# Optimization experiments

Measured on AMD Instinct MI355X. Metric: run time of the kernel, lower is better.

The kernel has to match this reference:

```python
import jax, jax.numpy as jnp
import numpy as np

NPERSEG = 512
STEP = 256
NSEG = 9            # frames for L=2048 with boundary='zeros', padded=True
NFREQ = 257
NUM_FILTER = 2
PI = 3.1415926      # same constant as source

_win = 0.5 * (1.0 - jnp.cos(2.0 * jnp.pi * jnp.arange(NPERSEG, dtype=jnp.float32) / NPERSEG))  # periodic hann (scipy get_window('hann'))
_win_sum = 256.0    # sum of periodic hann, exact


def _stft(x):
    # x: (B, D, L) real -> scipy.signal.stft(..., nperseg=512, noverlap=256) => (B, D, 257, 9)
    xp = jnp.pad(x, ((0, 0), (0, 0), (STEP, STEP)))  # boundary='zeros'
    idx = jnp.arange(NSEG)[:, None] * STEP + jnp.arange(NPERSEG)[None, :]
    frames = xp[..., idx] * _win                     # (B,D,9,512)
    Z = jnp.fft.rfft(frames, axis=-1) / _win_sum     # scaling='spectrum'
    return jnp.swapaxes(Z, -1, -2)                   # (B,D,257,9)


def _istft(Z):
    # Z: (B,D,257,9) complex -> (B,D,2048) real (scipy.signal.istft inverse)
    xs = jnp.fft.irfft(jnp.swapaxes(Z, -1, -2) * _win_sum, n=NPERSEG, axis=-1) * _win  # (B,D,9,512)
    total = NPERSEG + (NSEG - 1) * STEP  # 2560
    idx = (jnp.arange(NSEG)[:, None] * STEP + jnp.arange(NPERSEG)[None, :]).reshape(-1)
    B, D = Z.shape[0], Z.shape[1]
    x = jnp.zeros((B, D, total), xs.dtype).at[..., idx].add(xs.reshape(B, D, -1))
    norm = jnp.zeros((total,), jnp.float32).at[idx].add(jnp.tile(_win ** 2, NSEG))
    x = x / jnp.where(norm > 1e-10, norm, 1.0)
    return x[..., STEP:total - STEP]  # trim boundary padding -> length 2048


def _cplx(p):
    return p[..., 0] + 1j * p[..., 1]  # torch.view_as_complex


def _filter(x, length, bank):
    # x: (B,S,D) complex; bank: (K,S,D,2). power = x*x/length (complex square, as in source)
    power = x * x / length
    k = jnp.arange(NUM_FILTER, dtype=jnp.float32)
    coef = jnp.cos((2.0 * (k + 1.0) - 1.0) * PI / 2.0 * NUM_FILTER)  # matches source precedence
    return jnp.sum(power[None] * _cplx(bank)[:, None] * coef[:, None, None, None], axis=0)


def _ln(x, g, b):
    m = jnp.mean(x, -1, keepdims=True)
    v = jnp.mean((x - m) ** 2, -1, keepdims=True)
    return (x - m) * jax.lax.rsqrt(v + 1e-5) * g + b


def _addnorm(x, g1, b1, w1, bb1, w2, bb2, g2, b2):
    x = _ln(x, g1, b1)
    h = jax.nn.gelu(x @ w1.T + bb1, approximate=False)  # torch GELU (exact)
    return _ln(h @ w2.T + bb2 + x, g2, b2)


def setup_inputs() -> dict:
    key = jax.random.key(0)
    ks = jax.random.split(key, 12)
    B, D = 8, 768
    d = {}
    d['ecg'] = jax.random.normal(ks[0], (B, 2048, D), jnp.float32)
    d['image'] = jax.random.normal(ks[1], (B, 196, D), jnp.float32)
    d['ecg_filter_bank'] = jax.random.normal(ks[2], (2, 2313, D, 2), jnp.float32)
    d['cxr_filter_bank'] = jax.random.normal(ks[3], (2, 99, D, 2), jnp.float32)
    d['gate_sel'] = jax.random.normal(ks[4], (99, D, 2), jnp.float32)
    d['gate_w'] = jax.random.normal(ks[5], (D, D), jnp.float32) * 0.02
    d['gate_b'] = jnp.zeros((D,), jnp.float32)
    for i, p in enumerate(['e', 'c']):
        d[p + '_ln1_g'] = jnp.ones((D,), jnp.float32)
        d[p + '_ln1_b'] = jnp.zeros((D,), jnp.float32)
        d[p + '_w1'] = jax.random.normal(ks[6 + 2 * i], (D, D), jnp.float32) * 0.02
        d[p + '_b1'] = jnp.zeros((D,), jnp.float32)
        d[p + '_w2'] = jax.random.normal(ks[7 + 2 * i], (D, D), jnp.float32) * 0.02
        d[p + '_b2'] = jnp.zeros((D,), jnp.float32)
        d[p + '_ln2_g'] = jnp.ones((D,), jnp.float32)
        d[p + '_ln2_b'] = jnp.zeros((D,), jnp.float32)
    return d


def reference(ecg, image, ecg_filter_bank, cxr_filter_bank, gate_sel, gate_w, gate_b,
              e_ln1_g, e_ln1_b, e_w1, e_b1, e_w2, e_b2, e_ln2_g, e_ln2_b,
              c_ln1_g, c_ln1_b, c_w1, c_b1, c_w2, c_b2, c_ln2_g, c_ln2_b):
    B, S, D = ecg.shape
    N = image.shape[1]
    # STFT path (source detaches to CPU -> stop_gradient)
    Z = _stft(jnp.swapaxes(jax.lax.stop_gradient(ecg), 1, 2))       # (B,D,257,9)
    _ecg = jnp.transpose(Z, (0, 2, 3, 1)).reshape(B, NFREQ * NSEG, D)
    _img = jnp.fft.rfft(image, axis=1, norm='ortho')                # (B,99,D)
    _ecg = _filter(_ecg, NFREQ * NSEG, ecg_filter_bank)
    _img = _filter(_img, N // 2 + 1, cxr_filter_bank)
    # Cxr2EcgGate: complex selection, avgpool over spatial (real part), 1x1 conv
    gate = jnp.mean((_img * _cplx(gate_sel)).real, axis=1) @ gate_w.T + gate_b  # (B,D)
    ecg_g = _ecg * gate[:, None, :]
    # NOTE: source overwrites gated image with irfft of filtered _image (ecg_gate output unused)
    img_t = jnp.fft.irfft(_img, n=N, axis=1, norm='ortho')          # (B,N,D)
    Zg = jnp.transpose(ecg_g.reshape(B, NFREQ, NSEG, D), (0, 3, 1, 2))
    ecg_t = jnp.swapaxes(_istft(jax.lax.stop_gradient(Zg)), 1, 2)   # (B,2048,D); source detaches before istft
    text = _addnorm(ecg_t + ecg, e_ln1_g, e_ln1_b, e_w1, e_b1, e_w2, e_b2, e_ln2_g, e_ln2_b)
    img = _addnorm(img_t + image, c_ln1_g, c_ln1_b, c_w1, c_b1, c_w2, c_b2, c_ln2_g, c_ln2_b)
    return (text, img)
```

## Files before the change

### kernel.cpp

```cpp
#include <hip/hip_runtime.h>
#include <math.h>

namespace {

constexpr int B_ = 8;
constexpr int S_ = 2048;
constexpr int D_ = 768;
constexpr int N_ = 196;
constexpr int NF_ = 99;
constexpr int NFREQ_ = 257;
constexpr int NSEG_ = 9;
constexpr int NBINS_ = NFREQ_ * NSEG_;
constexpr int NW_ = D_ * D_;
constexpr float TWOPI_ = 6.28318530717958647692f;

using bf16x8 = __attribute__((ext_vector_type(8))) short;
using f32x4  = __attribute__((ext_vector_type(4))) float;

__device__ __forceinline__ int rev9(int x) { return (int)(__brev((unsigned)x) >> 23); }
__device__ __forceinline__ int padz(int i) { return i + (i >> 4); }

__device__ __forceinline__ unsigned short f2bf(float x) {
  unsigned u = __float_as_uint(x);
  u = (u + 0x7FFFu + ((u >> 16) & 1u)) >> 16;
  return (unsigned short)u;
}
__device__ __forceinline__ float bf2f(unsigned short h) {
  return __uint_as_float(((unsigned)h) << 16);
}

__device__ __forceinline__ float gelu_f(float v) {
  const float x = fabsf(v) * 0.70710678118654752440f;
  const float t = 1.0f / fmaf(0.3275911f, x, 1.0f);
  float p = fmaf(fmaf(fmaf(fmaf(1.061405429f, t, -1.453152027f), t, 1.421413741f),
                      t, -0.284496736f), t, 0.254829592f);
  const float e = __expf(-x * x);
  const float er = 1.0f - p * t * e;
  return 0.5f * v * (1.0f + ((v < 0.f) ? -er : er));
}

__device__ __forceinline__ void gload16(const void* g, void* l) {
  __builtin_amdgcn_global_load_lds((const __attribute__((address_space(1))) void*)g,
                                   (__attribute__((address_space(3))) void*)l, 16, 0, 0);
}

__device__ __forceinline__ float2 cmulf(float2 a, float2 b) {
  return make_float2(a.x * b.x - a.y * b.y, a.x * b.y + a.y * b.x);
}
__device__ __forceinline__ float2 cadd(float2 a, float2 b) {
  return make_float2(a.x + b.x, a.y + b.y);
}
__device__ __forceinline__ float2 csub(float2 a, float2 b) {
  return make_float2(a.x - b.x, a.y - b.y);
}

__global__ __launch_bounds__(256) void k_transpose_g(const float* __restrict__ src,
                                                     float* __restrict__ dst,
                                                     int R, int C) {
  __shared__ float tile[32][33];
  const int b = blockIdx.z;
  const int c0 = blockIdx.x * 32;
  const int r0 = blockIdx.y * 32;
  const int tx = threadIdx.x & 31, ty = threadIdx.x >> 5;
  for (int i = ty; i < 32; i += 8)
    tile[i][tx] = src[((size_t)b * R + r0 + i) * C + c0 + tx];
  __syncthreads();
  for (int i = ty; i < 32; i += 8)
    dst[((size_t)b * C + c0 + i) * R + r0 + tx] = tile[tx][i];
}

constexpr int PREP_W = (NW_ + 255) / 256;
constexpr int PREP_WALL = 4 * PREP_W;
__global__ __launch_bounds__(256) void k_prep(
    const float* __restrict__ w0, const float* __restrict__ w1,
    const float* __restrict__ w2, const float* __restrict__ w3,
    unsigned short* __restrict__ wbf, float2* __restrict__ twg,
    float2* __restrict__ twN) {
  const int bid = blockIdx.x;
  if (bid < PREP_WALL) {
    const int m = bid / PREP_W;
    const int i = (bid - m * PREP_W) * 256 + threadIdx.x;
    if (i >= NW_) return;
    const float* src = (m == 0) ? w0 : (m == 1) ? w1 : (m == 2) ? w2 : w3;
    wbf[(size_t)m * NW_ + i] = f2bf(src[i]);
  } else if (bid < PREP_WALL + 2) {
    const int i = (bid - PREP_WALL) * 256 + threadIdx.x;
    if (i >= 511) return;
    const int v = i + 1;
    const int h = 1 << (31 - __clz(v));
    const int j = v - h;
    float sn, cs;
    sincosf((float)j * ((TWOPI_ * 0.5f) / (float)h), &sn, &cs);
    twg[i] = make_float2(cs, sn);
  } else {
    const int i = threadIdx.x;
    if (i >= N_) return;
    float sn, cs;
    sincosf(TWOPI_ * (float)i / (float)N_, &sn, &cs);
    twN[i] = make_float2(cs, sn);
  }
}

__global__ __launch_bounds__(256) void k_fc_t(const float2* __restrict__ e2,
                                              float2* __restrict__ FcT) {
  __shared__ float2 tile[32][33];
  const int d0 = blockIdx.x * 32;
  const int k0 = blockIdx.y * 32;
  const int f = blockIdx.z;
  const int tx = threadIdx.x & 31, ty = threadIdx.x >> 5;
  for (int i = ty; i < 32; i += 8) {
    const int k = k0 + i;
    if (k < NFREQ_) {
      const size_t s = (size_t)(k * 9 + f) * D_ + d0 + tx;
      const float2 a = e2[s];
      const float2 b = e2[(size_t)NBINS_ * D_ + s];
      tile[i][tx] = make_float2(-(a.x + b.x), -(a.y + b.y));
    }
  }
  __syncthreads();
  const int k = k0 + tx;
  if (k < NFREQ_) {
    for (int i = ty; i < 32; i += 8)
      FcT[(size_t)(d0 + i) * NBINS_ + f * 257 + k] = tile[tx][i];
  }
}

__global__ __launch_bounds__(256) void k_img_dft_f(
    const float* __restrict__ image, const float2* __restrict__ bank2,
    const float2* __restrict__ gsel2, const float2* __restrict__ twN,
    float2* __restrict__ imgF, float* __restrict__ part) {
  const int fg = blockIdx.x;
  const int f0 = fg * 9;
  const int d = blockIdx.y * 256 + threadIdx.x;
  const int b = blockIdx.z;
  __shared__ float2 tws[9 * N_];
  for (int idx = threadIdx.x; idx < 9 * N_; idx += 256) {
    const int fi = idx / N_;
    const int t = idx - fi * N_;
    tws[idx] = twN[((f0 + fi) * t) % N_];
  }
  __syncthreads();
  float re[9] = {}, im[9] = {};
  const float* ip = image + (size_t)b * N_ * D_ + d;
  for (int t = 0; t < N_; ++t) {
    const float v = ip[(size_t)t * D_];
#pragma unroll
    for (int fi = 0; fi < 9; ++fi) {
      const float2 w = tws[fi * N_ + t];
      re[fi] = fmaf(v, w.x, re[fi]);
      im[fi] = fmaf(-v, w.y, im[fi]);
    }
  }
  const float sc = 1.0f / (196.0f * 99.0f);
  float gp = 0.f;
#pragma unroll
  for (int fi = 0; fi < 9; ++fi) {
    const int f = f0 + fi;
    const float pr = (re[fi] * re[fi] - im[fi] * im[fi]) * sc;
    const float pi2 = (2.f * re[fi] * im[fi]) * sc;
    const size_t fd = (size_t)f * D_ + d;
    const float2 c0 = bank2[fd];
    const float2 c1 = bank2[(size_t)NF_ * D_ + fd];
    const float fcr = -(c0.x + c1.x), fci = -(c0.y + c1.y);
    const float zr = pr * fcr - pi2 * fci;
    const float zi = pr * fci + pi2 * fcr;
    imgF[(size_t)(b * NF_ + f) * D_ + d] = make_float2(zr, zi);
    const float2 gw = gsel2[fd];
    gp += zr * gw.x - zi * gw.y;
  }
  part[((size_t)b * 11 + fg) * D_ + d] = gp;
}

__global__ __launch_bounds__(256) void k_gate_mm2(const float* __restrict__ part,
                                                  const float* __restrict__ W,
                                                  const float* __restrict__ bias,
                                                  float* __restrict__ gate) {
  __shared__ float row[8][D_];
  __shared__ float red[16][16][8];
  const int tid = threadIdx.x;
  const int d0 = blockIdx.x * 16;
  for (int i = tid; i < 8 * D_; i += 256) {
    const int b = i / D_, e = i - b * D_;
    float s = 0.f;
    for (int p = 0; p < 11; ++p) s += part[((size_t)b * 11 + p) * D_ + e];
    row[b][e] = s * (1.0f / 99.0f);
  }
  __syncthreads();
  const int dl = tid >> 4;
  const int ec = tid & 15;
  const float* w = W + (size_t)(d0 + dl) * D_ + ec * 48;
  float acc[8] = {};
  for (int e = 0; e < 48; e += 4) {
    const float4 wv = *reinterpret_cast<const float4*>(w + e);
    const int eg = ec * 48 + e;
#pragma unroll
    for (int b = 0; b < 8; ++b) {
      acc[b] = fmaf(row[b][eg], wv.x, acc[b]);
      acc[b] = fmaf(row[b][eg + 1], wv.y, acc[b]);
      acc[b] = fmaf(row[b][eg + 2], wv.z, acc[b]);
      acc[b] = fmaf(row[b][eg + 3], wv.w, acc[b]);
    }
  }
#pragma unroll
  for (int b = 0; b < 8; ++b) red[dl][ec][b] = acc[b];
  __syncthreads();
  if (tid < 128) {
    const int dl2 = tid >> 3, b = tid & 7;
    float s = bias[d0 + dl2];
    for (int c = 0; c < 16; ++c) s += red[dl2][c][b];
    gate[b * D_ + d0 + dl2] = s;
  }
}

__global__ __launch_bounds__(256) void k_img_idft(
    const float2* __restrict__ imgF, const float* __restrict__ image,
    const float2* __restrict__ twN, float* __restrict__ xi) {
  const int t0 = blockIdx.x * 14;
  const int d = blockIdx.y * 256 + threadIdx.x;
  const int b = blockIdx.z;
  __shared__ float2 tws[14 * NF_];
  for (int idx = threadIdx.x; idx < 14 * NF_; idx += 256) {
    const int ti = idx / NF_;
    const int f = idx - ti * NF_;
    tws[idx] = twN[((t0 + ti) * f) % N_];
  }
  __syncthreads();
  const float2* zp = imgF + (size_t)b * NF_ * D_ + d;
  const float2 z0 = zp[0];
  const float2 zny = zp[(size_t)(NF_ - 1) * D_];
  float acc[14];
#pragma unroll
  for (int ti = 0; ti < 14; ++ti)
    acc[ti] = z0.x + (((t0 + ti) & 1) ? -zny.x : zny.x);
  for (int f = 1; f < NF_ - 1; ++f) {
    const float2 z = zp[(size_t)f * D_];
#pragma unroll
    for (int ti = 0; ti < 14; ++ti) {
      const float2 w = tws[ti * NF_ + f];
      acc[ti] += 2.f * (z.x * w.x - z.y * w.y);
    }
  }
#pragma unroll
  for (int ti = 0; ti < 14; ++ti) {
    const size_t idx = (size_t)(b * N_ + t0 + ti) * D_ + d;
    xi[idx] = acc[ti] * (1.0f / 14.0f) + image[idx];
  }
}

__global__ __launch_bounds__(256) void k_layernorm_f2b(const float* __restrict__ x,
                                                       const float* __restrict__ g,
                                                       const float* __restrict__ b,
                                                       unsigned short* __restrict__ out) {
  const int row = blockIdx.x;
  const int tid = threadIdx.x;
  const float* xr = x + (size_t)row * D_;
  const float v0 = xr[tid], v1 = xr[tid + 256], v2 = xr[tid + 512];
  float s = v0 + v1 + v2;
  float q = v0 * v0 + v1 * v1 + v2 * v2;
  __shared__ float red[8];
  for (int off = 32; off > 0; off >>= 1) {
    s += __shfl_down(s, off);
    q += __shfl_down(q, off);
  }
  if ((tid & 63) == 0) { red[tid >> 6] = s; red[4 + (tid >> 6)] = q; }
  __syncthreads();
  s = red[0] + red[1] + red[2] + red[3];
  q = red[4] + red[5] + red[6] + red[7];
  const float mean = s * (1.0f / 768.0f);
  const float var = q * (1.0f / 768.0f) - mean * mean;
  const float inv = rsqrtf(var + 1e-5f);
  unsigned short* orow = out + (size_t)row * D_;
  orow[tid]       = f2bf((v0 - mean) * inv * g[tid]       + b[tid]);
  orow[tid + 256] = f2bf((v1 - mean) * inv * g[tid + 256] + b[tid + 256]);
  orow[tid + 512] = f2bf((v2 - mean) * inv * g[tid + 512] + b[tid + 512]);
}

template <int H, int DIR, bool TRIV>
__device__ __forceinline__ void pass8(float2* z, int l,
                                      float2 wa, float2 wb, float2 wc) {
  asm volatile("s_waitcnt lgkmcnt(0)" ::: "memory");
  const float sg = (DIR < 0) ? -1.f : 1.f;
  const int base = (H == 1) ? (l << 3)
                 : (H == 8) ? (((l >> 3) << 6) | (l & 7))
                            : l;
  const float2 x0 = z[padz(base)],         x1 = z[padz(base + H)];
  const float2 x2 = z[padz(base + 2 * H)], x3 = z[padz(base + 3 * H)];
  const float2 x4 = z[padz(base + 4 * H)], x5 = z[padz(base + 5 * H)];
  const float2 x6 = z[padz(base + 6 * H)], x7 = z[padz(base + 7 * H)];
  const float2 WA = make_float2(wa.x, sg * wa.y);
  const float2 WB = make_float2(wb.x, sg * wb.y);
  const float2 WC = make_float2(wc.x, sg * wc.y);
  const float2 WBp = make_float2(-sg * WB.y, sg * WB.x);
  float2 t, u;
  t = TRIV ? x1 : cmulf(x1, WA); const float2 A0 = cadd(x0, t), A1 = csub(x0, t);
  t = TRIV ? x3 : cmulf(x3, WA); const float2 A2 = cadd(x2, t), A3 = csub(x2, t);
  t = TRIV ? x5 : cmulf(x5, WA); const float2 A4 = cadd(x4, t), A5 = csub(x4, t);
  t = TRIV ? x7 : cmulf(x7, WA); const float2 A6 = cadd(x6, t), A7 = csub(x6, t);
  t = TRIV ? A2 : cmulf(A2, WB);
  u = TRIV ? make_float2(-sg * A3.y, sg * A3.x) : cmulf(A3, WBp);
  const float2 B0 = cadd(A0, t), B2 = csub(A0, t);
  const float2 B1 = cadd(A1, u), B3 = csub(A1, u);
  t = TRIV ? A6 : cmulf(A6, WB);
  u = TRIV ? make_float2(-sg * A7.y, sg * A7.x) : cmulf(A7, WBp);
  const float2 B4 = cadd(A4, t), B6 = csub(A4, t);
  const float2 B5 = cadd(A5, u), B7 = csub(A5, u);
  const float r_ = 0.70710678118654752440f;
  const float2 F1 = TRIV ? make_float2(r_, sg * r_)
                         : cmulf(WC, make_float2(r_, sg * r_));
  const float2 F2 = TRIV ? make_float2(0.f, sg)
                         : make_float2(-sg * WC.y, sg * WC.x);
  const float2 F3 = TRIV ? make_float2(-r_, sg * r_)
                         : cmulf(WC, make_float2(-r_, sg * r_));
  t = TRIV ? B4 : cmulf(B4, WC);
  z[padz(base)]         = cadd(B0, t);
  z[padz(base + 4 * H)] = csub(B0, t);
  t = cmulf(B5, F1);
  z[padz(base + H)]     = cadd(B1, t);
  z[padz(base + 5 * H)] = csub(B1, t);
  t = cmulf(B6, F2);
  z[padz(base + 2 * H)] = cadd(B2, t);
  z[padz(base + 6 * H)] = csub(B2, t);
  t = cmulf(B7, F3);
  z[padz(base + 3 * H)] = cadd(B3, t);
  z[padz(base + 7 * H)] = csub(B3, t);
}

template <int FA, int FB>
__device__ __forceinline__ void scatter_buf(float2* z, const float (&s)[8],
                                            float wlo, float whi, int rlo, int rhi) {
  constexpr int iAlo = (FA > 0) ? FA - 1 : 0;
  constexpr int iAhi = (FA < 8) ? FA : 0;
  constexpr int iBlo = (FB > 0) ? FB - 1 : 0;
  constexpr int iBhi = (FB >= 0 && FB < 8) ? FB : 0;
  const float aLo = (FA == 0) ? 0.f : s[iAlo] * wlo;
  const float aHi = (FA == 8) ? 0.f : s[iAhi] * whi;
  const float bLo = (FB <= 0) ? 0.f : s[iBlo] * wlo;
  const float bHi = (FB < 0 || FB == 8) ? 0.f : s[iBhi] * whi;
  z[rlo] = make_float2(aLo, bLo);
  z[rhi] = make_float2(aHi, bHi);
}

template <int FA, int FB>
__device__ __forceinline__ void filt_pack2(const float2* z, int k, float gA, float gB,
                                           float2 cA, float2 cB,
                                           float2& Ck, float2& Cm) {
  const int q = (512 - k) & 511;
  const float2 Zk = z[padz(k)], Zq = z[padz(q)];
  const float sc = 0.5f / 256.f;
  const float ar = (Zk.x + Zq.x) * sc, ai = (Zk.y - Zq.y) * sc;
  float yar, yai, ybr = 0.f, ybi = 0.f;
  {
    const float pr = (ar * ar - ai * ai) * (1.f / 2313.f);
    const float pi = (2.f * ar * ai) * (1.f / 2313.f);
    yar = (pr * cA.x - pi * cA.y) * gA;
    yai = (pr * cA.y + pi * cA.x) * gA;
  }
  if (FB >= 0) {
    const float br = (Zk.y + Zq.y) * sc, bi = (Zq.x - Zk.x) * sc;
    const float pr = (br * br - bi * bi) * (1.f / 2313.f);
    const float pi = (2.f * br * bi) * (1.f / 2313.f);
    ybr = (pr * cB.x - pi * cB.y) * gB;
    ybi = (pr * cB.y + pi * cB.x) * gB;
  }
  if (k == 0 || k == 256) {
    Ck = make_float2(yar, ybr);
    Cm = Ck;
  } else {
    Ck = make_float2(yar - ybi, yai + ybr);
    Cm = make_float2(yar + ybi, ybr - yai);
  }
}

template <int FA0, int FB0, int FA1, int FB1, int FA2, int FB2, int FA3, int FB3,
          int NBUF>
__device__ __forceinline__ void ecg_super4(int tid, float g,
                                           const float2* __restrict__ fc,
                                           const float (&s)[8], const float2 (&ptw)[6],
                                           float2 t8, float2* zA, float2* zB,
                                           float2* zC, float2* zD, float* accr) {
  const float c0 = t8.x;
  const float wlo = 0.5f - 0.5f * c0;
  const float whi = 0.5f + 0.5f * c0;
  float2 cA0 = fc[FA0 * 257 + tid];
  float2 cB0 = make_float2(0.f, 0.f), cA1 = cB0, cB1 = cB0;
  float2 cA2 = cB0, cB2 = cB0, cA3 = cB0, cB3 = cB0;
  if (FB0 >= 0) cB0 = fc[FB0 * 257 + tid];
  if (NBUF > 1) { cA1 = fc[FA1 * 257 + tid]; cB1 = fc[FB1 * 257 + tid]; }
  if (NBUF > 2) { cA2 = fc[FA2 * 257 + tid]; cB2 = fc[FB2 * 257 + tid]; }
  if (NBUF > 3) { cA3 = fc[FA3 * 257 + tid]; cB3 = fc[FB3 * 257 + tid]; }
  __syncthreads();
  const int rlo = padz(rev9(tid)), rhi = padz(rev9(tid + 256));
  scatter_buf<FA0, FB0>(zA, s, wlo, whi, rlo, rhi);
  if (NBUF > 1) scatter_buf<FA1, FB1>(zB, s, wlo, whi, rlo, rhi);
  if (NBUF > 2) scatter_buf<FA2, FB2>(zC, s, wlo, whi, rlo, rhi);
  if (NBUF > 3) scatter_buf<FA3, FB3>(zD, s, wlo, whi, rlo, rhi);
  __syncthreads();
  const int wid = tid >> 6, l = tid & 63;
  if (wid < NBUF) {
    float2* zz = (wid == 0) ? zA : (wid == 1) ? zB : (wid == 2) ? zC : zD;
    pass8<1, -1, true>(zz, l, ptw[0], ptw[1], ptw[2]);
    pass8<8, -1, false>(zz, l, ptw[0], ptw[1], ptw[2]);
    pass8<64, -1, false>(zz, l, ptw[3], ptw[4], ptw[5]);
  }
  __syncthreads();
  float2 Ck0, Cm0, Ck1, Cm1, Ck2, Cm2, Ck3, Cm3;
  float2 Cn0, Cn1, Cn2, Cn3, dum;
  filt_pack2<FA0, FB0>(zA, tid, g, g, cA0, cB0, Ck0, Cm0);
  if (NBUF > 1) filt_pack2<FA1, FB1>(zB, tid, g, g, cA1, cB1, Ck1, Cm1);
  if (NBUF > 2) filt_pack2<FA2, FB2>(zC, tid, g, g, cA2, cB2, Ck2, Cm2);
  if (NBUF > 3) filt_pack2<FA3, FB3>(zD, tid, g, g, cA3, cB3, Ck3, Cm3);
  if (tid == 0) {
    float2 nA, nB = make_float2(0.f, 0.f);
    nA = fc[FA0 * 257 + 256];
    if (FB0 >= 0) nB = fc[FB0 * 257 + 256];
    filt_pack2<FA0, FB0>(zA, 256, g, g, nA, nB, Cn0, dum);
    if (NBUF > 1) {
      nA = fc[FA1 * 257 + 256]; nB = fc[FB1 * 257 + 256];
      filt_pack2<FA1, FB1>(zB, 256, g, g, nA, nB, Cn1, dum);
    }
    if (NBUF > 2) {
      nA = fc[FA2 * 257 + 256]; nB = fc[FB2 * 257 + 256];
      filt_pack2<FA2, FB2>(zC, 256, g, g, nA, nB, Cn2, dum);
    }
    if (NBUF > 3) {
      nA = fc[FA3 * 257 + 256]; nB = fc[FB3 * 257 + 256];
      filt_pack2<FA3, FB3>(zD, 256, g, g, nA, nB, Cn3, dum);
    }
  }
  __syncthreads();
  {
    zA[rlo] = Ck0;
    if (NBUF > 1) zB[rlo] = Ck1;
    if (NBUF > 2) zC[rlo] = Ck2;
    if (NBUF > 3) zD[rlo] = Ck3;
    if (tid == 0) {
      zA[padz(1)] = Cn0;
      if (NBUF > 1) zB[padz(1)] = Cn1;
      if (NBUF > 2) zC[padz(1)] = Cn2;
      if (NBUF > 3) zD[padz(1)] = Cn3;
    } else {
      const int rm = padz(rev9(512 - tid));
      zA[rm] = Cm0;
      if (NBUF > 1) zB[rm] = Cm1;
      if (NBUF > 2) zC[rm] = Cm2;
      if (NBUF > 3) zD[rm] = Cm3;
    }
  }
  __syncthreads();
  if (wid < NBUF) {
    float2* zz = (wid == 0) ? zA : (wid == 1) ? zB : (wid == 2) ? zC : zD;
    pass8<1, 1, true>(zz, l, ptw[0], ptw[1], ptw[2]);
    pass8<8, 1, false>(zz, l, ptw[0], ptw[1], ptw[2]);
    pass8<64, 1, false>(zz, l, ptw[3], ptw[4], ptw[5]);
  }
  __syncthreads();
  {
    const float2 vLo = zA[padz(tid)], vHi = zA[padz(tid + 256)];
    accr[FA0] += 0.5f * wlo * vLo.x;
    accr[FA0 + 1] += 0.5f * whi * vHi.x;
    if (FB0 >= 0) {
      accr[FB0] += 0.5f * wlo * vLo.y;
      accr[FB0 + 1] += 0.5f * whi * vHi.y;
    }
    if (NBUF > 1) {
      const float2 uLo = zB[padz(tid)], uHi = zB[padz(tid + 256)];
      accr[FA1] += 0.5f * wlo * uLo.x;
      accr[FA1 + 1] += 0.5f * whi * uHi.x;
      accr[FB1] += 0.5f * wlo * uLo.y;
      accr[FB1 + 1] += 0.5f * whi * uHi.y;
    }
    if (NBUF > 2) {
      const float2 uLo = zC[padz(tid)], uHi = zC[padz(tid + 256)];
      accr[FA2] += 0.5f * wlo * uLo.x;
      accr[FA2 + 1] += 0.5f * whi * uHi.x;
      accr[FB2] += 0.5f * wlo * uLo.y;
      accr[FB2 + 1] += 0.5f * whi * uHi.y;
    }
    if (NBUF > 3) {
      const float2 uLo = zD[padz(tid)], uHi = zD[padz(tid + 256)];
      accr[FA3] += 0.5f * wlo * uLo.x;
      accr[FA3 + 1] += 0.5f * whi * uHi.x;
      accr[FB3] += 0.5f * wlo * uLo.y;
      accr[FB3 + 1] += 0.5f * whi * uHi.y;
    }
  }
}

__global__ __launch_bounds__(256) void k_ecg_fft(
    const float* __restrict__ ecgT, const float2* __restrict__ FcT,
    const float* __restrict__ gate, const float2* __restrict__ twg,
    unsigned short* __restrict__ xtT) {
  const int bp = blockIdx.x;
  const int b = bp / 384, dp = bp - (bp / 384) * 384;
  const int dX = 2 * dp;
  const int bdX = b * D_ + dX;
  const int tid = threadIdx.x;

  __shared__ float2 zA[544], zB[544], zC[544], zD[544];

  float sX[8], sY[8];
  const float* srcX = ecgT + (size_t)bdX * S_;
  const float* srcY = srcX + S_;
#pragma unroll
  for (int k = 0; k < 8; ++k) { sX[k] = srcX[k * 256 + tid]; sY[k] = srcY[k * 256 + tid]; }

  const int l6 = tid & 63;
  float2 ptw[6];
  ptw[0] = twg[7 + (l6 & 7)];
  ptw[1] = twg[15 + (l6 & 7)];
  ptw[2] = twg[31 + (l6 & 7)];
  ptw[3] = twg[63 + l6];
  ptw[4] = twg[127 + l6];
  ptw[5] = twg[255 + l6];
  const float2 t8 = twg[255 + tid];
  const float c0 = t8.x;
  const float wlo = 0.5f - 0.5f * c0;
  const float whi = 0.5f + 0.5f * c0;
  const int rlo = padz(rev9(tid)), rhi = padz(rev9(tid + 256));

  const float gX = gate[bdX];
  const float gY = gate[bdX + 1];
  const float2* fcX = FcT + (size_t)dX * NBINS_;
  const float2* fcY = fcX + NBINS_;

  float accX[10], accY[10];
#pragma unroll
  for (int i = 0; i < 10; ++i) { accX[i] = 0.f; accY[i] = 0.f; }

  ecg_super4<0, 8, 1, 2, 3, 4, 5, 6, 4>(tid, gX, fcX, sX, ptw, t8, zA, zB, zC, zD, accX);
  ecg_super4<0, 8, 1, 2, 3, 4, 5, 6, 4>(tid, gY, fcY, sY, ptw, t8, zA, zB, zC, zD, accY);

  __syncthreads();
  zA[rlo] = make_float2(sX[6] * wlo, sY[6] * wlo);
  zA[rhi] = make_float2(sX[7] * whi, sY[7] * whi);
  __syncthreads();
  const int wid = tid >> 6, l = tid & 63;
  if (wid == 0) {
    pass8<1, -1, true>(zA, l, ptw[0], ptw[1], ptw[2]);
    pass8<8, -1, false>(zA, l, ptw[0], ptw[1], ptw[2]);
    pass8<64, -1, false>(zA, l, ptw[3], ptw[4], ptw[5]);
  }
  __syncthreads();
  float2 CkC, CmC, CnC, dum;
  {
    const float2 cA = fcX[7 * 257 + tid];
    const float2 cB = fcY[7 * 257 + tid];
    filt_pack2<7, 7>(zA, tid, gX, gY, cA, cB, CkC, CmC);
    if (tid == 0) {
      const float2 nA = fcX[7 * 257 + 256];
      const float2 nB = fcY[7 * 257 + 256];
      filt_pack2<7, 7>(zA, 256, gX, gY, nA, nB, CnC, dum);
    }
  }
  __syncthreads();
  {
    zA[rlo] = CkC;
    if (tid == 0) zA[padz(1)] = CnC;
    else zA[padz(rev9(512 - tid))] = CmC;
  }
  __syncthreads();
  if (wid == 0) {
    pass8<1, 1, true>(zA, l, ptw[0], ptw[1], ptw[2]);
    pass8<8, 1, false>(zA, l, ptw[0], ptw[1], ptw[2]);
    pass8<64, 1, false>(zA, l, ptw[3], ptw[4], ptw[5]);
  }
  __syncthreads();
  {
    const float2 vLo = zA[padz(tid)], vHi = zA[padz(tid + 256)];
    accX[7] += 0.5f * wlo * vLo.x;
    accX[8] += 0.5f * whi * vHi.x;
    accY[7] += 0.5f * wlo * vLo.y;
    accY[8] += 0.5f * whi * vHi.y;
  }

  const float rinv = 1.0f / (0.5f + 0.5f * c0 * c0);
  unsigned short* dstX = xtT + (size_t)bdX * S_;
  unsigned short* dstY = dstX + S_;
#pragma unroll
  for (int i2 = 0; i2 < 8; ++i2) {
    dstX[i2 * 256 + tid] = f2bf(accX[i2 + 1] * rinv + sX[i2]);
    dstY[i2 * 256 + tid] = f2bf(accY[i2 + 1] * rinv + sY[i2]);
  }
}

__global__ __launch_bounds__(256) void k_colstats_bf(const unsigned short* __restrict__ xtT,
                                                     float2* __restrict__ stats) {
  const int b = blockIdx.y;
  const int t0 = blockIdx.x * 128;
  const int tx = threadIdx.x & 63;
  const int ty = threadIdx.x >> 6;
  float s0 = 0.f, q0 = 0.f, s1 = 0.f, q1 = 0.f;
  const unsigned int* base = (const unsigned int*)(xtT + (size_t)b * D_ * S_);
  for (int dd = ty; dd < D_; dd += 4) {
    const unsigned int u = base[(size_t)dd * (S_ / 2) + (t0 >> 1) + tx];
    const float v0 = bf2f((unsigned short)(u & 0xffffu));
    const float v1 = bf2f((unsigned short)(u >> 16));
    s0 += v0; q0 = fmaf(v0, v0, q0);
    s1 += v1; q1 = fmaf(v1, v1, q1);
  }
  __shared__ float sh[4][64][4];
  sh[ty][tx][0] = s0; sh[ty][tx][1] = q0; sh[ty][tx][2] = s1; sh[ty][tx][3] = q1;
  __syncthreads();
  if (ty == 0) {
    s0 = sh[0][tx][0] + sh[1][tx][0] + sh[2][tx][0] + sh[3][tx][0];
    q0 = sh[0][tx][1] + sh[1][tx][1] + sh[2][tx][1] + sh[3][tx][1];
    s1 = sh[0][tx][2] + sh[1][tx][2] + sh[2][tx][2] + sh[3][tx][2];
    q1 = sh[0][tx][3] + sh[1][tx][3] + sh[2][tx][3] + sh[3][tx][3];
    stats[(size_t)b * S_ + t0 + 2 * tx]     = make_float2(s0, q0);
    stats[(size_t)b * S_ + t0 + 2 * tx + 1] = make_float2(s1, q1);
  }
}

__global__ __launch_bounds__(256) void k_transpose_ln(
    const unsigned short* __restrict__ xtT, const float2* __restrict__ stats,
    const float* __restrict__ g, const float* __restrict__ bia,
    unsigned short* __restrict__ xhat) {
  __shared__ float tile[32][33];
  const int b = blockIdx.z;
  const int t0 = blockIdx.x * 32;
  const int d0 = blockIdx.y * 32;
  const int tx = threadIdx.x & 31, ty = threadIdx.x >> 5;
  for (int i = ty; i < 32; i += 8)
    tile[i][tx] = bf2f(xtT[((size_t)b * D_ + d0 + i) * S_ + t0 + tx]);
  __syncthreads();
  const float gv = g[d0 + tx], bv = bia[d0 + tx];
  for (int i = ty; i < 32; i += 8) {
    const float2 st = stats[(size_t)b * S_ + t0 + i];
    const float mean = st.x * (1.0f / 768.0f);
    const float var = st.y * (1.0f / 768.0f) - mean * mean;
    const float inv = rsqrtf(var + 1e-5f);
    xhat[((size_t)b * S_ + t0 + i) * D_ + d0 + tx] =
        f2bf((tile[tx][i] - mean) * inv * gv + bv);
  }
}

__global__ __launch_bounds__(256) void k_layernorm_dual(
    const unsigned short* __restrict__ x1, const float* __restrict__ g1,
    const float* __restrict__ b1, float* __restrict__ o1, int n1,
    const unsigned short* __restrict__ x2, const float* __restrict__ g2,
    const float* __restrict__ b2, float* __restrict__ o2) {
  int row = blockIdx.x;
  const unsigned short* x; const float *g, *b; float* o;
  if (row < n1) { x = x1; g = g1; b = b1; o = o1; }
  else { row -= n1; x = x2; g = g2; b = b2; o = o2; }
  const int tid = threadIdx.x;
  const unsigned short* xr = x + (size_t)row * D_;
  const float v0 = bf2f(xr[tid]), v1 = bf2f(xr[tid + 256]), v2 = bf2f(xr[tid + 512]);
  float s = v0 + v1 + v2;
  float q = v0 * v0 + v1 * v1 + v2 * v2;
  __shared__ float red[8];
  for (int off = 32; off > 0; off >>= 1) {
    s += __shfl_down(s, off);
    q += __shfl_down(q, off);
  }
  if ((tid & 63) == 0) { red[tid >> 6] = s; red[4 + (tid >> 6)] = q; }
  __syncthreads();
  s = red[0] + red[1] + red[2] + red[3];
  q = red[4] + red[5] + red[6] + red[7];
  const float mean = s * (1.0f / 768.0f);
  const float var = q * (1.0f / 768.0f) - mean * mean;
  const float inv = rsqrtf(var + 1e-5f);
  float* orow = o + (size_t)row * D_;
  orow[tid]       = (v0 - mean) * inv * g[tid]       + b[tid];
  orow[tid + 256] = (v1 - mean) * inv * g[tid + 256] + b[tid + 256];
  orow[tid + 512] = (v2 - mean) * inv * g[tid + 512] + b[tid + 512];
}

template <int MODE>
__global__ __launch_bounds__(256) void k_gemm_dual(
    const unsigned short* __restrict__ A1, const unsigned short* __restrict__ W1,
    const float* __restrict__ b1, const unsigned short* __restrict__ r1,
    unsigned short* __restrict__ o1, int M1, int nby1,
    const unsigned short* __restrict__ A2, const unsigned short* __restrict__ W2,
    const float* __restrict__ b2, const unsigned short* __restrict__ r2,
    unsigned short* __restrict__ o2, int M2) {
  __shared__ unsigned short Asm[2][128 * 64];
  __shared__ unsigned short Bsm[2][128 * 64];
  const int tid = threadIdx.x;
  const int lane = tid & 63, wid = tid >> 6;
  const int wr = wid >> 1, wc = wid & 1;
  int bx, by;
  {
    const int nwg = gridDim.x * gridDim.y;
    const int bid = blockIdx.y * gridDim.x + blockIdx.x;
    const int xcd = bid & 7, lin = bid >> 3;
    const int qq = nwg >> 3, rr = nwg & 7;
    const int nbid = (xcd < rr) ? xcd * (qq + 1) + lin
                                : rr * (qq + 1) + (xcd - rr) * qq + lin;
    bx = nbid % gridDim.x;
    by = nbid / gridDim.x;
  }
  const unsigned short* Abf; const unsigned short* Wbf; const float* bias;
  const unsigned short* resid; unsigned short* outb; int M;
  if (by < nby1) { Abf = A1; Wbf = W1; bias = b1; resid = r1; outb = o1; M = M1; }
  else { by -= nby1; Abf = A2; Wbf = W2; bias = b2; resid = r2; outb = o2; M = M2; }
  const int n0 = bx * 128, m0 = by * 128;

  auto STAGE = [&](int buf, int kt) {
    const int k0 = kt * 64;
#pragma unroll
    for (int i = 0; i < 4; ++i) {
      const int c = tid + 256 * i;
      const int row = c >> 3, sl = c & 7;
      const int gsl = sl ^ (row & 7);
      gload16(Abf + (size_t)(m0 + row) * 768 + k0 + gsl * 8, &Asm[buf][c * 8]);
      gload16(Wbf + (size_t)(n0 + row) * 768 + k0 + gsl * 8, &Bsm[buf][c * 8]);
    }
  };

  f32x4 acc[4][4] = {};
  STAGE(0, 0);
  for (int kt = 0; kt < 12; ++kt) {
    const int cur = kt & 1;
    if (kt < 11) {
      STAGE(cur ^ 1, kt + 1);
      asm volatile("s_waitcnt vmcnt(8)" ::: "memory");
    } else {
      asm volatile("s_waitcnt vmcnt(0)" ::: "memory");
    }
    __builtin_amdgcn_sched_barrier(0);
    __builtin_amdgcn_s_barrier();
#pragma unroll
    for (int ks = 0; ks < 2; ++ks) {
      bf16x8 af[4], bfv[4];
#pragma unroll
      for (int mi = 0; mi < 4; ++mi) {
        const int row = wr * 64 + mi * 16 + (lane & 15);
        const int sl = (ks * 4 + (lane >> 4)) ^ (row & 7);
        af[mi] = *(const bf16x8*)((const char*)Asm[cur] + row * 128 + sl * 16);
      }
#pragma unroll
      for (int ni = 0; ni < 4; ++ni) {
        const int row = wc * 64 + ni * 16 + (lane & 15);
        const int sl = (ks * 4 + (lane >> 4)) ^ (row & 7);
        bfv[ni] = *(const bf16x8*)((const char*)Bsm[cur] + row * 128 + sl * 16);
      }
#pragma unroll
      for (int mi = 0; mi < 4; ++mi)
#pragma unroll
        for (int ni = 0; ni < 4; ++ni)
          acc[mi][ni] = __builtin_amdgcn_mfma_f32_16x16x32_bf16(af[mi], bfv[ni],
                                                                acc[mi][ni], 0, 0, 0);
    }
    __builtin_amdgcn_sched_barrier(0);
    __builtin_amdgcn_s_barrier();
  }
#pragma unroll
  for (int mi = 0; mi < 4; ++mi) {
#pragma unroll
    for (int ni = 0; ni < 4; ++ni) {
      const int col = n0 + wc * 64 + ni * 16 + (lane & 15);
#pragma unroll
      for (int e = 0; e < 4; ++e) {
        const int row = m0 + wr * 64 + mi * 16 + (lane >> 4) * 4 + e;
        if (row >= M) continue;
        float v = acc[mi][ni][e] + bias[col];
        if (MODE == 0) {
          v = gelu_f(v);
        } else {
          v += bf2f(resid[(size_t)row * 768 + col]);
        }
        outb[(size_t)row * 768 + col] = f2bf(v);
      }
    }
  }
}

}

extern "C" void kernel_launch(void* const* d_in, const int* in_sizes, int n_in,
                              void* d_out, int out_size, void* d_ws, size_t ws_size,
                              hipStream_t stream) {
  (void)in_sizes; (void)n_in; (void)out_size; (void)ws_size;
  const float* ecg     = (const float*)d_in[0];
  const float* image   = (const float*)d_in[1];
  const float* ebank   = (const float*)d_in[2];
  const float* cbank   = (const float*)d_in[3];
  const float* gsel    = (const float*)d_in[4];
  const float* gw      = (const float*)d_in[5];
  const float* gb      = (const float*)d_in[6];
  const float* e_ln1_g = (const float*)d_in[7];
  const float* e_ln1_b = (const float*)d_in[8];
  const float* e_w1    = (const float*)d_in[9];
  const float* e_b1    = (const float*)d_in[10];
  const float* e_w2    = (const float*)d_in[11];
  const float* e_b2    = (const float*)d_in[12];
  const float* e_ln2_g = (const float*)d_in[13];
  const float* e_ln2_b = (const float*)d_in[14];
  const float* c_ln1_g = (const float*)d_in[15];
  const float* c_ln1_b = (const float*)d_in[16];
  const float* c_w1    = (const float*)d_in[17];
  const float* c_b1    = (const float*)d_in[18];
  const float* c_w2    = (const float*)d_in[19];
  const float* c_b2    = (const float*)d_in[20];
  const float* c_ln2_g = (const float*)d_in[21];
  const float* c_ln2_b = (const float*)d_in[22];

  float* out = (float*)d_out;
  float* ws = (float*)d_ws;

  constexpr size_t TXT = (size_t)8 * 2048 * 768;
  constexpr size_t IMG = (size_t)8 * 196 * 768;

  float* A  = ws;
  float* Bb = A + TXT;
  unsigned short* wbf = (unsigned short*)(Bb + TXT);
  unsigned short* ew1b = wbf;
  unsigned short* ew2b = wbf + NW_;
  unsigned short* cw1b = wbf + 2 * NW_;
  unsigned short* cw2b = wbf + 3 * NW_;
  float* gatev = (float*)(wbf + 4 * (size_t)NW_);
  float2* stats = (float2*)(gatev + 8 * 768);
  float* gpart = (float*)(stats + 8 * 2048);
  float2* twg = (float2*)(gpart + 8 * 11 * 768);
  float2* twN = twg + 511;

  float2* FcT = (float2*)out;

  unsigned short* xhat = (unsigned short*)A;
  unsigned short* y_tb = (unsigned short*)A + TXT;
  unsigned short* xtT = (unsigned short*)Bb;
  unsigned short* h_t = (unsigned short*)Bb;
  float* Bb2 = Bb + TXT / 2;
  float2* imgF = (float2*)Bb2;
  float* xi = Bb2 + 1216512;
  unsigned short* xh_i = (unsigned short*)(xi + IMG);
  unsigned short* h_i  = xh_i + IMG;
  unsigned short* y_ib = h_i + IMG;

  k_prep<<<PREP_WALL + 3, 256, 0, stream>>>(e_w1, e_w2, c_w1, c_w2, wbf, twg, twN);
  k_fc_t<<<dim3(24, 9, 9), 256, 0, stream>>>((const float2*)ebank, FcT);

  k_img_dft_f<<<dim3(11, 3, 8), 256, 0, stream>>>(image, (const float2*)cbank,
                                                  (const float2*)gsel, twN, imgF, gpart);
  k_gate_mm2<<<48, 256, 0, stream>>>(gpart, gw, gb, gatev);
  k_img_idft<<<dim3(14, 3, 8), 256, 0, stream>>>(imgF, image, twN, xi);
  k_layernorm_f2b<<<1568, 256, 0, stream>>>(xi, c_ln1_g, c_ln1_b, xh_i);

  k_transpose_g<<<dim3(24, 64, 8), 256, 0, stream>>>(ecg, A, 2048, 768);
  k_ecg_fft<<<3072, 256, 0, stream>>>(A, FcT, gatev, twg, xtT);
  k_colstats_bf<<<dim3(16, 8), 256, 0, stream>>>(xtT, stats);
  k_transpose_ln<<<dim3(64, 24, 8), 256, 0, stream>>>(xtT, stats, e_ln1_g, e_ln1_b, xhat);

  k_gemm_dual<0><<<dim3(6, 141), 256, 0, stream>>>(
      xhat, ew1b, e_b1, nullptr, h_t, 16384, 128,
      xh_i, cw1b, c_b1, nullptr, h_i, 1568);
  k_gemm_dual<1><<<dim3(6, 141), 256, 0, stream>>>(
      h_t, ew2b, e_b2, xhat, y_tb, 16384, 128,
      h_i, cw2b, c_b2, xh_i, y_ib, 1568);
  k_layernorm_dual<<<16384 + 1568, 256, 0, stream>>>(
      y_tb, e_ln2_g, e_ln2_b, out, 16384,
      y_ib, c_ln2_g, c_ln2_b, out + TXT);
}
```

Before: 390.8 us.

## Enlarge GEMM block tile to 256x128 with 512 threads, single-buffered LDS

Each dual GEMM workgroup now covers 256 rows instead of 128, using 8 waves in a 4x2 arrangement, so each weight tile loaded into LDS is reused across twice as many rows. The double-buffered LDS pipeline and its explicit vmcnt waits are replaced by a single buffer with __syncthreads around the stage of the next K tile. This roughly halves the grid and cuts total LDS use. The cost is that global loads no longer overlap MFMA work, and the image GEMM's last tile reads further past the valid row count.

```diff
diff --git a/kernel.cpp b/kernel.cpp
--- a/kernel.cpp
+++ b/kernel.cpp
@@ -667,15 +667,15 @@
 }
 
 template <int MODE>
-__global__ __launch_bounds__(256) void k_gemm_dual(
+__global__ __launch_bounds__(512) void k_gemm_dual(
     const unsigned short* __restrict__ A1, const unsigned short* __restrict__ W1,
     const float* __restrict__ b1, const unsigned short* __restrict__ r1,
     unsigned short* __restrict__ o1, int M1, int nby1,
     const unsigned short* __restrict__ A2, const unsigned short* __restrict__ W2,
     const float* __restrict__ b2, const unsigned short* __restrict__ r2,
     unsigned short* __restrict__ o2, int M2) {
-  __shared__ unsigned short Asm[2][128 * 64];
-  __shared__ unsigned short Bsm[2][128 * 64];
+  __shared__ unsigned short Asm[256 * 64];
+  __shared__ unsigned short Bsm[128 * 64];
   const int tid = threadIdx.x;
   const int lane = tid & 63, wid = tid >> 6;
   const int wr = wid >> 1, wc = wid & 1;
@@ -694,32 +694,30 @@
   const unsigned short* resid; unsigned short* outb; int M;
   if (by < nby1) { Abf = A1; Wbf = W1; bias = b1; resid = r1; outb = o1; M = M1; }
   else { by -= nby1; Abf = A2; Wbf = W2; bias = b2; resid = r2; outb = o2; M = M2; }
-  const int n0 = bx * 128, m0 = by * 128;
-
-  auto STAGE = [&](int buf, int kt) {
+  const int n0 = bx * 128, m0 = by * 256;
+
+  auto STAGE = [&](int kt) {
     const int k0 = kt * 64;
 #pragma unroll
     for (int i = 0; i < 4; ++i) {
-      const int c = tid + 256 * i;
+      const int c = tid + 512 * i;
       const int row = c >> 3, sl = c & 7;
       const int gsl = sl ^ (row & 7);
-      gload16(Abf + (size_t)(m0 + row) * 768 + k0 + gsl * 8, &Asm[buf][c * 8]);
-      gload16(Wbf + (size_t)(n0 + row) * 768 + k0 + gsl * 8, &Bsm[buf][c * 8]);
+      gload16(Abf + (size_t)(m0 + row) * 768 + k0 + gsl * 8, &Asm[c * 8]);
+    }
+#pragma unroll
+    for (int i = 0; i < 2; ++i) {
+      const int c = tid + 512 * i;
+      const int row = c >> 3, sl = c & 7;
+      const int gsl = sl ^ (row & 7);
+      gload16(Wbf + (size_t)(n0 + row) * 768 + k0 + gsl * 8, &Bsm[c * 8]);
     }
   };
 
   f32x4 acc[4][4] = {};
-  STAGE(0, 0);
+  STAGE(0);
   for (int kt = 0; kt < 12; ++kt) {
-    const int cur = kt & 1;
-    if (kt < 11) {
-      STAGE(cur ^ 1, kt + 1);
-      asm volatile("s_waitcnt vmcnt(8)" ::: "memory");
-    } else {
-      asm volatile("s_waitcnt vmcnt(0)" ::: "memory");
-    }
-    __builtin_amdgcn_sched_barrier(0);
-    __builtin_amdgcn_s_barrier();
+    __syncthreads();
 #pragma unroll
     for (int ks = 0; ks < 2; ++ks) {
       bf16x8 af[4], bfv[4];
@@ -727,13 +725,13 @@
       for (int mi = 0; mi < 4; ++mi) {
         const int row = wr * 64 + mi * 16 + (lane & 15);
         const int sl = (ks * 4 + (lane >> 4)) ^ (row & 7);
-        af[mi] = *(const bf16x8*)((const char*)Asm[cur] + row * 128 + sl * 16);
+        af[mi] = *(const bf16x8*)((const char*)Asm + row * 128 + sl * 16);
       }
 #pragma unroll
       for (int ni = 0; ni < 4; ++ni) {
         const int row = wc * 64 + ni * 16 + (lane & 15);
         const int sl = (ks * 4 + (lane >> 4)) ^ (row & 7);
-        bfv[ni] = *(const bf16x8*)((const char*)Bsm[cur] + row * 128 + sl * 16);
+        bfv[ni] = *(const bf16x8*)((const char*)Bsm + row * 128 + sl * 16);
       }
 #pragma unroll
       for (int mi = 0; mi < 4; ++mi)
@@ -742,8 +740,10 @@
           acc[mi][ni] = __builtin_amdgcn_mfma_f32_16x16x32_bf16(af[mi], bfv[ni],
                                                                 acc[mi][ni], 0, 0, 0);
     }
-    __builtin_amdgcn_sched_barrier(0);
-    __builtin_amdgcn_s_barrier();
+    if (kt < 11) {
+      __syncthreads();
+      STAGE(kt + 1);
+    }
   }
 #pragma unroll
   for (int mi = 0; mi < 4; ++mi) {
@@ -842,11 +842,11 @@
   k_colstats_bf<<<dim3(16, 8), 256, 0, stream>>>(xtT, stats);
   k_transpose_ln<<<dim3(64, 24, 8), 256, 0, stream>>>(xtT, stats, e_ln1_g, e_ln1_b, xhat);
 
-  k_gemm_dual<0><<<dim3(6, 141), 256, 0, stream>>>(
-      xhat, ew1b, e_b1, nullptr, h_t, 16384, 128,
+  k_gemm_dual<0><<<dim3(6, 71), 512, 0, stream>>>(
+      xhat, ew1b, e_b1, nullptr, h_t, 16384, 64,
       xh_i, cw1b, c_b1, nullptr, h_i, 1568);
-  k_gemm_dual<1><<<dim3(6, 141), 256, 0, stream>>>(
-      h_t, ew2b, e_b2, xhat, y_tb, 16384, 128,
+  k_gemm_dual<1><<<dim3(6, 71), 512, 0, stream>>>(
+      h_t, ew2b, e_b2, xhat, y_tb, 16384, 64,
       h_i, cw2b, c_b2, xh_i, y_ib, 1568);
   k_layernorm_dual<<<16384 + 1568, 256, 0, stream>>>(
       y_tb, e_ln2_g, e_ln2_b, out, 16384,
```

After: 396.7 us. About the same (+1.5%).
